# Kernel optimization log

Measured on AMD Instinct MI355X. Metric: run time of the kernel, lower is better.

## Reference

```python
import jax, jax.numpy as jnp
import numpy as np

ENCODER_DIM = 2048
DECODER_DIM = 512
ATTENTION_DIM = 512
BATCH = 512
NUM_PIXELS = 196


def setup_inputs() -> dict:
    key = jax.random.key(0)
    k = jax.random.split(key, 8)
    s_e = 1.0 / np.sqrt(ENCODER_DIM)
    s_d = 1.0 / np.sqrt(DECODER_DIM)
    s_a = 1.0 / np.sqrt(ATTENTION_DIM)
    return {
        "encoder_out": jax.random.normal(k[0], (BATCH, NUM_PIXELS, ENCODER_DIM), jnp.float32),
        "decoder_hidden": jax.random.normal(k[1], (BATCH, DECODER_DIM), jnp.float32),
        "W_enc": jax.random.uniform(k[2], (ENCODER_DIM, ATTENTION_DIM), jnp.float32, -s_e, s_e),
        "b_enc": jax.random.uniform(k[3], (ATTENTION_DIM,), jnp.float32, -s_e, s_e),
        "W_dec": jax.random.uniform(k[4], (DECODER_DIM, ATTENTION_DIM), jnp.float32, -s_d, s_d),
        "b_dec": jax.random.uniform(k[5], (ATTENTION_DIM,), jnp.float32, -s_d, s_d),
        "W_full": jax.random.uniform(k[6], (ATTENTION_DIM,), jnp.float32, -s_a, s_a),
        "b_full": jax.random.uniform(k[7], (), jnp.float32, -s_a, s_a),
    }


def reference(encoder_out, decoder_hidden, W_enc, b_enc, W_dec, b_dec, W_full, b_full):
    # att1: [B, P, A], att2: [B, A]
    att1 = jnp.einsum('bpe,ea->bpa', encoder_out, W_enc) + b_enc
    att2 = decoder_hidden @ W_dec + b_dec
    # scores: [B, P]
    scores = jnp.einsum('bpa,a->bp', jnp.tanh(att1 + att2[:, None, :]), W_full) + b_full
    alpha = jax.nn.softmax(scores, axis=1)
    context = jnp.einsum('bpe,bp->be', encoder_out, alpha)
    return context, alpha
```

## Files before the change

kernel.cpp:

```cpp
#include <hip/hip_runtime.h>
#include <hip/hip_bf16.h>
#include <stdint.h>

#define BATCH 512
#define PIX   196
#define EDIM  2048
#define DDIM  512
#define ADIM  512
#define MROWS (BATCH*PIX)

#define BM 128
#define BN 128
#define BK 32
#define NT (EDIM/BK)

typedef __attribute__((ext_vector_type(8))) short bf16x8;
typedef __attribute__((ext_vector_type(8))) float f32x8;
typedef __attribute__((ext_vector_type(8))) __bf16 bf16v8;
typedef __attribute__((ext_vector_type(4))) float f32x4;

#define GLL16(g, lptr) __builtin_amdgcn_global_load_lds( \
    (const __attribute__((address_space(1))) void*)(g),  \
    (__attribute__((address_space(3))) void*)(lptr), 16, 0, 0)

static __device__ __forceinline__ unsigned short f2bf(float f) {
  union { float f; uint32_t u; } v; v.f = f;
  uint32_t u = v.u;
  return (unsigned short)((u + 0x7FFFu + ((u >> 16) & 1u)) >> 16);
}

static __device__ __forceinline__ float bf2f(unsigned short u) {
  union { uint32_t u; float f; } v; v.u = ((uint32_t)u) << 16;
  return v.f;
}

static __device__ __forceinline__ bf16x8 cvt8(float4 a, float4 b) {
  f32x8 v = {a.x, a.y, a.z, a.w, b.x, b.y, b.z, b.w};
  bf16v8 c = __builtin_convertvector(v, bf16v8);
  bf16x8 r;
  __builtin_memcpy(&r, &c, 16);
  return r;
}

__global__ void k_transpose_wenc(const float* __restrict__ W,
                                 unsigned short* __restrict__ Bt) {
  __shared__ float tile[32][33];
  const int kt = blockIdx.x;
  const int nt = blockIdx.y;
  const int tx = threadIdx.x, ty = threadIdx.y;
#pragma unroll
  for (int j = 0; j < 4; j++)
    tile[ty + 8*j][tx] = W[(size_t)(kt*32 + ty + 8*j)*ADIM + nt*32 + tx];
  __syncthreads();
#pragma unroll
  for (int j = 0; j < 4; j++)
    Bt[(size_t)(nt*32 + ty + 8*j)*EDIM + kt*32 + tx] = f2bf(tile[tx][ty + 8*j]);
}

__global__ void k_att2(const float* __restrict__ H, const float* __restrict__ Wd,
                       const float* __restrict__ bd, float* __restrict__ att2) {
  __shared__ float h[DDIM];
  const int b = blockIdx.x;
  const int t = threadIdx.x;
  h[t]       = H[(size_t)b*DDIM + t];
  h[t + 256] = H[(size_t)b*DDIM + t + 256];
  __syncthreads();
  float a0 = 0.f, a1 = 0.f;
#pragma unroll 8
  for (int k = 0; k < DDIM; k++) {
    const float hv = h[k];
    a0 += hv * Wd[(size_t)k*ADIM + t];
    a1 += hv * Wd[(size_t)k*ADIM + t + 256];
  }
  att2[(size_t)b*ADIM + t]       = a0 + bd[t];
  att2[(size_t)b*ADIM + t + 256] = a1 + bd[t + 256];
}

__global__ __launch_bounds__(256) void k_preconvert(const float* __restrict__ in,
                                                    unsigned short* __restrict__ out,
                                                    long n8) {
  long i = (long)blockIdx.x * 256 + threadIdx.x;
  const long stride = (long)gridDim.x * 256;
  for (; i < n8; i += stride) {
    const float4* p = (const float4*)(in + i*8);
    const float4 a = p[0], b = p[1];
    *(bf16x8*)(out + i*8) = cvt8(a, b);
  }
}

__global__ __launch_bounds__(256, 3) void k_gemm_bf16(
    const unsigned short* __restrict__ At,
    const unsigned short* __restrict__ Bt,
    const float* __restrict__ b_enc,
    const float* __restrict__ att2,
    const float* __restrict__ W_full,
    float* __restrict__ scores)
{
  __shared__ __align__(16) char ldsA[2*8192];
  __shared__ __align__(16) char ldsB[2*8192];

  const int t   = threadIdx.x;
  const int l   = t & 63;
  const int wid = t >> 6;
  const int wr  = wid >> 1;
  const int wc  = wid & 1;

  const int orig = blockIdx.x;
  const int tile = (orig & 7) * 392 + (orig >> 3);
  const int bm0 = (tile >> 2) * BM;
  const int bn0 = (tile & 3) * BN;

  const int r0 = t >> 2, c0 = t & 3;
  const unsigned short* srcA0 = At + (size_t)(bm0 + r0      ) * EDIM + ((c0 ^ (r0 & 3)) * 8);
  const unsigned short* srcA1 = At + (size_t)(bm0 + r0 + 64 ) * EDIM + ((c0 ^ (r0 & 3)) * 8);
  const unsigned short* srcB0 = Bt + (size_t)(bn0 + r0      ) * EDIM + ((c0 ^ (r0 & 3)) * 8);
  const unsigned short* srcB1 = Bt + (size_t)(bn0 + r0 + 64 ) * EDIM + ((c0 ^ (r0 & 3)) * 8);
  const int d0 = wid * 1024;
  const int d1 = 4096 + wid * 1024;

  const int l15 = l & 15, hi = l >> 4;
  const int ck  = (hi ^ (l15 & 3)) * 16;
  const int baseA = wr*4096 + l15*64 + ck;
  const int baseB = wc*4096 + l15*64 + ck;

  f32x4 acc[4][4] = {};

#define STG(BUF, KT) do {                                        \
    GLL16(srcA0 + (size_t)(KT)*BK, ldsA + (BUF)*8192 + d0);      \
    GLL16(srcA1 + (size_t)(KT)*BK, ldsA + (BUF)*8192 + d1);      \
    GLL16(srcB0 + (size_t)(KT)*BK, ldsB + (BUF)*8192 + d0);      \
    GLL16(srcB1 + (size_t)(KT)*BK, ldsB + (BUF)*8192 + d1);      \
  } while (0)

#define CMP(BUF) do {                                            \
    bf16x8 af[4], bfr[4];                                        \
    _Pragma("unroll")                                            \
    for (int ni = 0; ni < 4; ni++)                               \
      bfr[ni] = *(const bf16x8*)(ldsB + (BUF)*8192 + ni*1024 + baseB); \
    _Pragma("unroll")                                            \
    for (int mi = 0; mi < 4; mi++)                               \
      af[mi] = *(const bf16x8*)(ldsA + (BUF)*8192 + mi*1024 + baseA); \
    _Pragma("unroll")                                            \
    for (int mi = 0; mi < 4; mi++)                               \
      _Pragma("unroll")                                          \
      for (int ni = 0; ni < 4; ni++)                             \
        acc[mi][ni] = __builtin_amdgcn_mfma_f32_16x16x32_bf16(   \
            af[mi], bfr[ni], acc[mi][ni], 0, 0, 0);              \
  } while (0)

  STG(0, 0);
  __syncthreads();
  for (int kt = 0; kt < NT; kt += 2) {
    STG(1, kt + 1);
    CMP(0);
    __syncthreads();
    if (kt + 2 < NT) STG(0, kt + 2);
    CMP(1);
    __syncthreads();
  }

  float be[4], wf[4];
  int colv[4];
#pragma unroll
  for (int ni = 0; ni < 4; ni++) {
    colv[ni] = bn0 + wc*64 + ni*16 + l15;
    be[ni] = b_enc[colv[ni]];
    wf[ni] = W_full[colv[ni]];
  }
#pragma unroll
  for (int mi = 0; mi < 4; mi++) {
#pragma unroll
    for (int e = 0; e < 4; e++) {
      const int row_l = wr*64 + mi*16 + hi*4 + e;
      const unsigned gr = (unsigned)(bm0 + row_l);
      const unsigned b  = gr / 196u;
      float s = 0.f;
#pragma unroll
      for (int ni = 0; ni < 4; ni++) {
        const float v = acc[mi][ni][e] + be[ni] + att2[(size_t)b*ADIM + colv[ni]];
        s += tanhf(v) * wf[ni];
      }
      s += __shfl_xor(s, 1); s += __shfl_xor(s, 2);
      s += __shfl_xor(s, 4); s += __shfl_xor(s, 8);
      if (l15 == 0) atomicAdd(&scores[gr], s);
    }
  }
}

__global__ void k_softmax(float* __restrict__ sa) {
  __shared__ float red[256];
  const int b = blockIdx.x, t = threadIdx.x;
  const float v = (t < PIX) ? sa[(size_t)b*PIX + t] : -1e30f;
  red[t] = v; __syncthreads();
  for (int s2 = 128; s2 > 0; s2 >>= 1) {
    if (t < s2) red[t] = fmaxf(red[t], red[t + s2]);
    __syncthreads();
  }
  const float m = red[0]; __syncthreads();
  const float e = (t < PIX) ? __expf(v - m) : 0.f;
  red[t] = e; __syncthreads();
  for (int s2 = 128; s2 > 0; s2 >>= 1) {
    if (t < s2) red[t] += red[t + s2];
    __syncthreads();
  }
  const float inv = 1.f / red[0];
  if (t < PIX) sa[(size_t)b*PIX + t] = e * inv;
}

__global__ __launch_bounds__(256) void k_context_bf16(
    const unsigned short* __restrict__ encbf, const float* __restrict__ alpha,
    float* __restrict__ ctx) {
  __shared__ float al[PIX];
  const int b = blockIdx.x, t = threadIdx.x;
  if (t < PIX) al[t] = alpha[(size_t)b*PIX + t];
  __syncthreads();
  const unsigned short* e = encbf + (size_t)b * PIX * EDIM + t * 8;
  float acc[8] = {};
  for (int p = 0; p < PIX; p++) {
    const bf16x8 v = *(const bf16x8*)(e + (size_t)p * EDIM);
    const float a = al[p];
#pragma unroll
    for (int j = 0; j < 8; j++)
      acc[j] += a * bf2f((unsigned short)v[j]);
  }
  float4 o0 = {acc[0], acc[1], acc[2], acc[3]};
  float4 o1 = {acc[4], acc[5], acc[6], acc[7]};
  float4* dst = (float4*)(ctx + (size_t)b * EDIM + t * 8);
  dst[0] = o0; dst[1] = o1;
}

__global__ __launch_bounds__(256, 3) void k_gemm_scores(
    const float* __restrict__ enc, const unsigned short* __restrict__ Bt,
    const float* __restrict__ b_enc, const float* __restrict__ att2,
    const float* __restrict__ W_full, float* __restrict__ scores) {
  __shared__ __align__(16) char ldsA[2*8192];
  __shared__ __align__(16) char ldsB[3*8192];
  const int t = threadIdx.x, l = t & 63, wid = t >> 6;
  const int wr = wid >> 1, wc = wid & 1;
  const int orig = blockIdx.x;
  const int tile = (orig & 7) * 392 + (orig >> 3);
  const int bm0 = (tile >> 2) * BM, bn0 = (tile & 3) * BN;
  const int arow = t >> 1;
  const float* srcA = enc + (size_t)(bm0 + arow) * EDIM + (t & 1) * 16;
  const int g0 = (t & 1) * 2;
  const int wA0 = arow*64 + (((g0    ) ^ (arow & 3)) * 16);
  const int wA1 = arow*64 + (((g0 + 1) ^ (arow & 3)) * 16);
  const unsigned short* srcB[2];
#pragma unroll
  for (int j = 0; j < 2; j++) {
    const int idx = j*256 + t; const int row = idx >> 2;
    srcB[j] = Bt + (size_t)(bn0 + row) * EDIM + ((idx & 3) ^ (row & 3)) * 8;
  }
  const int dB = wid * 1024;
  const int l15 = l & 15, hi = l >> 4;
  const int ck = (hi ^ (l15 & 3)) * 16;
  const int baseA = wr*4096 + l15*64 + ck;
  const int baseB = wc*4096 + l15*64 + ck;
  float4 ar[2][4];
  f32x4 acc[4][4] = {};
#define F_A_ISSUE(SLOT, KT) do { const float* _s = srcA + (size_t)(KT) * BK; \
    ar[SLOT][0] = *(const float4*)(_s); ar[SLOT][1] = *(const float4*)(_s + 4); \
    ar[SLOT][2] = *(const float4*)(_s + 8); ar[SLOT][3] = *(const float4*)(_s + 12); } while (0)
#define F_B_GLL(BUF, KT) do { \
    GLL16(srcB[0] + (size_t)(KT)*BK, ldsB + (BUF)*8192 + dB); \
    GLL16(srcB[1] + (size_t)(KT)*BK, ldsB + (BUF)*8192 + 4096 + dB); } while (0)
#define F_A_WRITE(LBUF, SLOT) do { \
    bf16x8 w0 = cvt8(ar[SLOT][0], ar[SLOT][1]); bf16x8 w1 = cvt8(ar[SLOT][2], ar[SLOT][3]); \
    *(bf16x8*)(ldsA + (LBUF)*8192 + wA0) = w0; *(bf16x8*)(ldsA + (LBUF)*8192 + wA1) = w1; } while (0)
#define F_COMPUTE(BA, BB) do { bf16x8 af[4], bfr[4]; \
    _Pragma("unroll") for (int ni = 0; ni < 4; ni++) \
      bfr[ni] = *(const bf16x8*)(ldsB + (BB)*8192 + ni*1024 + baseB); \
    _Pragma("unroll") for (int mi = 0; mi < 4; mi++) \
      af[mi] = *(const bf16x8*)(ldsA + (BA)*8192 + mi*1024 + baseA); \
    _Pragma("unroll") for (int mi = 0; mi < 4; mi++) \
      _Pragma("unroll") for (int ni = 0; ni < 4; ni++) \
        acc[mi][ni] = __builtin_amdgcn_mfma_f32_16x16x32_bf16(af[mi], bfr[ni], acc[mi][ni], 0, 0, 0); } while (0)
#define F_TILE(T, CUR, BB, BBS) do { F_A_ISSUE(CUR, (T)+2); F_B_GLL(BBS, (T)+2); \
    F_COMPUTE(CUR, BB); asm volatile("s_waitcnt vmcnt(6)" ::: "memory"); \
    F_A_WRITE((CUR)^1, (CUR)^1); asm volatile("s_waitcnt lgkmcnt(0)" ::: "memory"); \
    __builtin_amdgcn_s_barrier(); } while (0)
  F_A_ISSUE(0, 0); F_B_GLL(0, 0); F_A_ISSUE(1, 1); F_B_GLL(1, 1);
  asm volatile("s_waitcnt vmcnt(8)" ::: "memory");
  F_A_WRITE(0, 0);
  asm volatile("s_waitcnt vmcnt(6) lgkmcnt(0)" ::: "memory");
  __builtin_amdgcn_s_barrier();
  for (int kb = 0; kb < 60; kb += 6) {
    F_TILE(kb+0, 0, 0, 2); F_TILE(kb+1, 1, 1, 0); F_TILE(kb+2, 0, 2, 1);
    F_TILE(kb+3, 1, 0, 2); F_TILE(kb+4, 0, 1, 0); F_TILE(kb+5, 1, 2, 1);
  }
  F_TILE(60, 0, 0, 2); F_TILE(61, 1, 1, 0);
  { F_COMPUTE(0, 2); asm volatile("s_waitcnt vmcnt(2)" ::: "memory");
    F_A_WRITE(1, 1); asm volatile("s_waitcnt vmcnt(0) lgkmcnt(0)" ::: "memory");
    __builtin_amdgcn_s_barrier(); }
  F_COMPUTE(1, 0);
  float be[4], wf[4]; int colv[4];
#pragma unroll
  for (int ni = 0; ni < 4; ni++) {
    colv[ni] = bn0 + wc*64 + ni*16 + l15;
    be[ni] = b_enc[colv[ni]]; wf[ni] = W_full[colv[ni]];
  }
#pragma unroll
  for (int mi = 0; mi < 4; mi++) {
#pragma unroll
    for (int e = 0; e < 4; e++) {
      const int row_l = wr*64 + mi*16 + hi*4 + e;
      const unsigned gr = (unsigned)(bm0 + row_l);
      const unsigned b  = gr / 196u;
      float s = 0.f;
#pragma unroll
      for (int ni = 0; ni < 4; ni++) {
        const float v = acc[mi][ni][e] + be[ni] + att2[(size_t)b*ADIM + colv[ni]];
        s += tanhf(v) * wf[ni];
      }
      s += __shfl_xor(s, 1); s += __shfl_xor(s, 2);
      s += __shfl_xor(s, 4); s += __shfl_xor(s, 8);
      if (l15 == 0) atomicAdd(&scores[gr], s);
    }
  }
}

__global__ __launch_bounds__(512) void k_context(
    const float* __restrict__ enc, const float* __restrict__ alpha,
    float* __restrict__ ctx) {
  __shared__ float al[PIX];
  const int b = blockIdx.x, t = threadIdx.x;
  if (t < PIX) al[t] = alpha[(size_t)b*PIX + t];
  __syncthreads();
  const float4* e4 = (const float4*)(enc + (size_t)b * PIX * EDIM);
  float4 acc = {0.f, 0.f, 0.f, 0.f};
#pragma unroll 4
  for (int p = 0; p < PIX; p++) {
    const float4 v = e4[(size_t)p * (EDIM/4) + t];
    const float a = al[p];
    acc.x += v.x * a; acc.y += v.y * a; acc.z += v.z * a; acc.w += v.w * a;
  }
  ((float4*)(ctx + (size_t)b * EDIM))[t] = acc;
}

extern "C" void kernel_launch(void* const* d_in, const int* in_sizes, int n_in,
                              void* d_out, int out_size, void* d_ws, size_t ws_size,
                              hipStream_t stream) {
  (void)in_sizes; (void)n_in; (void)out_size;
  const float* enc   = (const float*)d_in[0];
  const float* hid   = (const float*)d_in[1];
  const float* Wenc  = (const float*)d_in[2];
  const float* benc  = (const float*)d_in[3];
  const float* Wdec  = (const float*)d_in[4];
  const float* bdec  = (const float*)d_in[5];
  const float* Wfull = (const float*)d_in[6];

  float* ctx   = (float*)d_out;
  float* alpha = (float*)d_out + (size_t)BATCH * EDIM;

  const size_t encbf_b = (size_t)MROWS * EDIM * 2;
  const size_t bt_b    = (size_t)ADIM * EDIM * 2;
  const size_t att2_b  = (size_t)BATCH * ADIM * 4;

  if (ws_size >= encbf_b + bt_b + att2_b) {
    unsigned short* encbf = (unsigned short*)d_ws;
    unsigned short* Bt    = (unsigned short*)((char*)d_ws + encbf_b);
    float*          att2  = (float*)((char*)d_ws + encbf_b + bt_b);

    hipMemsetAsync(alpha, 0, (size_t)MROWS * sizeof(float), stream);
    k_transpose_wenc<<<dim3(64, 16), dim3(32, 8), 0, stream>>>(Wenc, Bt);
    k_att2<<<BATCH, 256, 0, stream>>>(hid, Wdec, bdec, att2);
    k_preconvert<<<2048, 256, 0, stream>>>(enc, encbf, (long)MROWS * EDIM / 8);
    k_gemm_bf16<<<3136, 256, 0, stream>>>(encbf, Bt, benc, att2, Wfull, alpha);
    k_softmax<<<BATCH, 256, 0, stream>>>(alpha);
    k_context_bf16<<<BATCH, 256, 0, stream>>>(encbf, alpha, ctx);
  } else {
    unsigned short* Bt   = (unsigned short*)d_ws;
    float*          att2 = (float*)((char*)d_ws + bt_b);

    hipMemsetAsync(alpha, 0, (size_t)MROWS * sizeof(float), stream);
    k_transpose_wenc<<<dim3(64, 16), dim3(32, 8), 0, stream>>>(Wenc, Bt);
    k_att2<<<BATCH, 256, 0, stream>>>(hid, Wdec, bdec, att2);
    k_gemm_scores<<<3136, 256, 0, stream>>>(enc, Bt, benc, att2, Wfull, alpha);
    k_softmax<<<BATCH, 256, 0, stream>>>(alpha);
    k_context<<<BATCH, 512, 0, stream>>>(enc, alpha, ctx);
  }
}
```

Baseline: 683.2 us.

## Replace 4-wave block GEMM with single-wave 64x64 tiles and register-loaded B

The bf16 score GEMM now runs one wave per 64x64 output tile instead of four waves on 128x128 tiles. A is triple-buffered in LDS through direct global-to-LDS loads, while B fragments are read straight from global memory into double-buffered registers. The K loop synchronises only with explicit vmcnt waits rather than block barriers. This removes __syncthreads stalls and adds prefetch depth, but each tile now reuses less data, so global and L2 traffic for B and A rise, and the hand-tuned vmcnt counts are fragile.

```diff
diff --git a/kernel.cpp b/kernel.cpp
--- a/kernel.cpp
+++ b/kernel.cpp
@@ -9,10 +9,7 @@
 #define ADIM  512
 #define MROWS (BATCH*PIX)
 
-#define BM 128
-#define BN 128
 #define BK 32
-#define NT (EDIM/BK)
 
 typedef __attribute__((ext_vector_type(8))) short bf16x8;
 typedef __attribute__((ext_vector_type(8))) float f32x8;
@@ -88,7 +85,7 @@
   }
 }
 
-__global__ __launch_bounds__(256, 3) void k_gemm_bf16(
+__global__ __launch_bounds__(64, 3) void k_gemm_wave(
     const unsigned short* __restrict__ At,
     const unsigned short* __restrict__ Bt,
     const float* __restrict__ b_enc,
@@ -96,74 +93,88 @@
     const float* __restrict__ W_full,
     float* __restrict__ scores)
 {
-  __shared__ __align__(16) char ldsA[2*8192];
-  __shared__ __align__(16) char ldsB[2*8192];
+  __shared__ __align__(16) char ldsA[3*4096];
 
   const int t   = threadIdx.x;
-  const int l   = t & 63;
-  const int wid = t >> 6;
-  const int wr  = wid >> 1;
-  const int wc  = wid & 1;
+  const int l15 = t & 15, hi = t >> 4;
 
   const int orig = blockIdx.x;
-  const int tile = (orig & 7) * 392 + (orig >> 3);
-  const int bm0 = (tile >> 2) * BM;
-  const int bn0 = (tile & 3) * BN;
-
-  const int r0 = t >> 2, c0 = t & 3;
-  const unsigned short* srcA0 = At + (size_t)(bm0 + r0      ) * EDIM + ((c0 ^ (r0 & 3)) * 8);
-  const unsigned short* srcA1 = At + (size_t)(bm0 + r0 + 64 ) * EDIM + ((c0 ^ (r0 & 3)) * 8);
-  const unsigned short* srcB0 = Bt + (size_t)(bn0 + r0      ) * EDIM + ((c0 ^ (r0 & 3)) * 8);
-  const unsigned short* srcB1 = Bt + (size_t)(bn0 + r0 + 64 ) * EDIM + ((c0 ^ (r0 & 3)) * 8);
-  const int d0 = wid * 1024;
-  const int d1 = 4096 + wid * 1024;
-
-  const int l15 = l & 15, hi = l >> 4;
-  const int ck  = (hi ^ (l15 & 3)) * 16;
-  const int baseA = wr*4096 + l15*64 + ck;
-  const int baseB = wc*4096 + l15*64 + ck;
-
+  const int lin  = (orig & 7) * 1568 + (orig >> 3);
+  const int bm0  = (lin >> 3) * 64;
+  const int bn0  = (lin & 7) * 64;
+
+  const unsigned short* srcA[4];
+#pragma unroll
+  for (int j = 0; j < 4; j++) {
+    const int r = j*16 + (t >> 2);
+    srcA[j] = At + (size_t)(bm0 + r)*EDIM + (((t & 3) ^ ((r >> 1) & 3)) * 8);
+  }
+  const unsigned short* pB[4];
+#pragma unroll
+  for (int ni = 0; ni < 4; ni++)
+    pB[ni] = Bt + (size_t)(bn0 + ni*16 + l15)*EDIM + hi*8;
+
+  const int addrA0 = l15*64 + ((hi ^ ((l15 >> 1) & 3)) * 16);
+
+  bf16x8 b[2][4];
   f32x4 acc[4][4] = {};
 
-#define STG(BUF, KT) do {                                        \
-    GLL16(srcA0 + (size_t)(KT)*BK, ldsA + (BUF)*8192 + d0);      \
-    GLL16(srcA1 + (size_t)(KT)*BK, ldsA + (BUF)*8192 + d1);      \
-    GLL16(srcB0 + (size_t)(KT)*BK, ldsB + (BUF)*8192 + d0);      \
-    GLL16(srcB1 + (size_t)(KT)*BK, ldsB + (BUF)*8192 + d1);      \
+#define W_GLLA(BUF, KT) do {                                     \
+    GLL16(srcA[0] + (size_t)(KT)*BK, ldsA + (BUF)*4096 + 0*1024);\
+    GLL16(srcA[1] + (size_t)(KT)*BK, ldsA + (BUF)*4096 + 1*1024);\
+    GLL16(srcA[2] + (size_t)(KT)*BK, ldsA + (BUF)*4096 + 2*1024);\
+    GLL16(srcA[3] + (size_t)(KT)*BK, ldsA + (BUF)*4096 + 3*1024);\
   } while (0)
 
-#define CMP(BUF) do {                                            \
-    bf16x8 af[4], bfr[4];                                        \
-    _Pragma("unroll")                                            \
-    for (int ni = 0; ni < 4; ni++)                               \
-      bfr[ni] = *(const bf16x8*)(ldsB + (BUF)*8192 + ni*1024 + baseB); \
+#define W_BLOAD(S, KT) do {                                      \
+    b[S][0] = *(const bf16x8*)(pB[0] + (size_t)(KT)*BK);         \
+    b[S][1] = *(const bf16x8*)(pB[1] + (size_t)(KT)*BK);         \
+    b[S][2] = *(const bf16x8*)(pB[2] + (size_t)(KT)*BK);         \
+    b[S][3] = *(const bf16x8*)(pB[3] + (size_t)(KT)*BK);         \
+  } while (0)
+
+#define W_CMP(BUF, S) do {                                       \
+    bf16x8 af[4];                                                \
     _Pragma("unroll")                                            \
     for (int mi = 0; mi < 4; mi++)                               \
-      af[mi] = *(const bf16x8*)(ldsA + (BUF)*8192 + mi*1024 + baseA); \
+      af[mi] = *(const bf16x8*)(ldsA + (BUF)*4096 + mi*1024 + addrA0); \
     _Pragma("unroll")                                            \
     for (int mi = 0; mi < 4; mi++)                               \
       _Pragma("unroll")                                          \
       for (int ni = 0; ni < 4; ni++)                             \
         acc[mi][ni] = __builtin_amdgcn_mfma_f32_16x16x32_bf16(   \
-            af[mi], bfr[ni], acc[mi][ni], 0, 0, 0);              \
+            af[mi], b[S][ni], acc[mi][ni], 0, 0, 0);             \
   } while (0)
 
-  STG(0, 0);
-  __syncthreads();
-  for (int kt = 0; kt < NT; kt += 2) {
-    STG(1, kt + 1);
-    CMP(0);
-    __syncthreads();
-    if (kt + 2 < NT) STG(0, kt + 2);
-    CMP(1);
-    __syncthreads();
-  }
+#define W_TILE(T) do {                                           \
+    W_BLOAD(((T)+1)&1, (T)+1);                                   \
+    W_GLLA(((T)+2)%3, (T)+2);                                    \
+    asm volatile("s_waitcnt vmcnt(12)" ::: "memory");            \
+    W_CMP((T)%3, (T)&1);                                         \
+  } while (0)
+
+  W_GLLA(0, 0);
+  W_GLLA(1, 1);
+  W_BLOAD(0, 0);
+  asm volatile("s_waitcnt vmcnt(8)" ::: "memory");
+
+  for (int kb = 0; kb < 60; kb += 6) {
+    W_TILE(kb+0); W_TILE(kb+1); W_TILE(kb+2);
+    W_TILE(kb+3); W_TILE(kb+4); W_TILE(kb+5);
+  }
+  W_TILE(60);
+  W_TILE(61);
+  W_BLOAD(1, 63);
+  asm volatile("s_waitcnt vmcnt(8)" ::: "memory");
+  W_CMP(2, 0);
+  asm volatile("s_waitcnt vmcnt(0)" ::: "memory");
+  W_CMP(0, 1);
 
   float be[4], wf[4];
   int colv[4];
 #pragma unroll
   for (int ni = 0; ni < 4; ni++) {
-    colv[ni] = bn0 + wc*64 + ni*16 + l15;
+    colv[ni] = bn0 + ni*16 + l15;
     be[ni] = b_enc[colv[ni]];
     wf[ni] = W_full[colv[ni]];
   }
@@ -171,13 +182,13 @@
   for (int mi = 0; mi < 4; mi++) {
 #pragma unroll
     for (int e = 0; e < 4; e++) {
-      const int row_l = wr*64 + mi*16 + hi*4 + e;
+      const int row_l = mi*16 + hi*4 + e;
       const unsigned gr = (unsigned)(bm0 + row_l);
-      const unsigned b  = gr / 196u;
+      const unsigned bb = gr / 196u;
       float s = 0.f;
 #pragma unroll
       for (int ni = 0; ni < 4; ni++) {
-        const float v = acc[mi][ni][e] + be[ni] + att2[(size_t)b*ADIM + colv[ni]];
+        const float v = acc[mi][ni][e] + be[ni] + att2[(size_t)bb*ADIM + colv[ni]];
         s += tanhf(v) * wf[ni];
       }
       s += __shfl_xor(s, 1); s += __shfl_xor(s, 2);
@@ -229,6 +240,8 @@
   dst[0] = o0; dst[1] = o1;
 }
 
+#define BM 128
+#define BN 128
 __global__ __launch_bounds__(256, 3) void k_gemm_scores(
     const float* __restrict__ enc, const unsigned short* __restrict__ Bt,
     const float* __restrict__ b_enc, const float* __restrict__ att2,
@@ -365,7 +378,7 @@
     k_transpose_wenc<<<dim3(64, 16), dim3(32, 8), 0, stream>>>(Wenc, Bt);
     k_att2<<<BATCH, 256, 0, stream>>>(hid, Wdec, bdec, att2);
     k_preconvert<<<2048, 256, 0, stream>>>(enc, encbf, (long)MROWS * EDIM / 8);
-    k_gemm_bf16<<<3136, 256, 0, stream>>>(encbf, Bt, benc, att2, Wfull, alpha);
+    k_gemm_wave<<<12544, 64, 0, stream>>>(encbf, Bt, benc, att2, Wfull, alpha);
     k_softmax<<<BATCH, 256, 0, stream>>>(alpha);
     k_context_bf16<<<BATCH, 256, 0, stream>>>(encbf, alpha, ctx);
   } else {
```

Result: slower. 922.1 us (+35.0%).
